# Kernel optimization log

Measured on AMD Instinct MI355X. Metric: run time of the kernel, lower is better.

Reference implementation:

```python
import jax, jax.numpy as jnp
import numpy as np

D_MODEL = 512
N_HEADS = 8
HEAD_DIM = D_MODEL // N_HEADS
SEQ = 2048
BATCH = 2
EPS = 1e-5
SCALE = 1.0 / np.sqrt(HEAD_DIM).astype(np.float32)
# (kind, window, dilation) per head, matching init_kwargs head_specs
SPECS = [("global", 0, 1), ("global", 0, 1),
         ("window", 64, 1), ("window", 128, 1), ("window", 256, 1),
         ("dilated", 64, 2), ("dilated", 64, 4), ("dilated", 64, 8)]


def build_masks(N):
    i = jnp.arange(N)
    D = jnp.abs(i[:, None] - i[None, :])
    ms = []
    for kind, w, dil in SPECS:
        if kind == "global":
            ms.append(jnp.ones((N, N), dtype=bool))
        elif kind == "window":
            ms.append(D <= w)
        else:  # dilated
            ms.append((D % dil == 0) & (D // dil <= w))
    return jnp.stack(ms)  # [H, N, N] bool


def layernorm(x, g, b):
    mu = jnp.mean(x, axis=-1, keepdims=True)
    var = jnp.mean((x - mu) ** 2, axis=-1, keepdims=True)
    return (x - mu) * jax.lax.rsqrt(var + EPS) * g + b


def setup_inputs() -> dict:
    key = jax.random.key(0)
    ks = jax.random.split(key, 7)
    w = 0.02
    return {
        "x": jax.random.normal(ks[0], (BATCH, SEQ, D_MODEL), dtype=jnp.float32),
        "Wq": jax.random.normal(ks[1], (D_MODEL, D_MODEL), dtype=jnp.float32) * w,
        "Wk": jax.random.normal(ks[2], (D_MODEL, D_MODEL), dtype=jnp.float32) * w,
        "Wv": jax.random.normal(ks[3], (D_MODEL, D_MODEL), dtype=jnp.float32) * w,
        "Wo": jax.random.normal(ks[4], (D_MODEL, D_MODEL), dtype=jnp.float32) * w,
        "T_w1": jax.random.normal(ks[5], (D_MODEL, D_MODEL), dtype=jnp.float32) * w,
        "T_b1": jnp.zeros((D_MODEL,), dtype=jnp.float32),
        "T_w2": jax.random.normal(ks[6], (1, D_MODEL), dtype=jnp.float32) * w,
        "T_b2": jnp.zeros((1,), dtype=jnp.float32),
        "ln_in_g": jnp.ones((D_MODEL,), dtype=jnp.float32),
        "ln_in_b": jnp.zeros((D_MODEL,), dtype=jnp.float32),
        "ln_out_g": jnp.ones((D_MODEL,), dtype=jnp.float32),
        "ln_out_b": jnp.zeros((D_MODEL,), dtype=jnp.float32),
    }


def reference(x, Wq, Wk, Wv, Wo, T_w1, T_b1, T_w2, T_b2,
              ln_in_g, ln_in_b, ln_out_g, ln_out_b):
    B, N, H = x.shape
    x0 = x
    xn = layernorm(x, ln_in_g, ln_in_b)
    # torch Linear: y = x @ W.T ; reshape to [B, h, N, d]
    def heads(W):
        return (xn @ W.T).reshape(B, N, N_HEADS, HEAD_DIM).transpose(0, 2, 1, 3)
    Q, K, V = heads(Wq), heads(Wk), heads(Wv)
    attn = jnp.einsum("bhqd,bhkd->bhqk", Q, K) * SCALE
    mask = build_masks(N)  # [h, N, N]
    attn = jnp.where(mask[None], attn, -jnp.inf)
    attn = jax.nn.softmax(attn, axis=-1)  # every row has diagonal unmasked
    out = jnp.einsum("bhqk,bhkd->bhqd", attn, V)
    out = out.transpose(0, 2, 1, 3).reshape(B, N, N_HEADS * HEAD_DIM)
    out = out @ Wo.T
    # tanh-gated softmax over sequence dim
    T_logits = jnp.tanh(xn @ T_w1.T + T_b1) @ T_w2.T + T_b2  # [B, N, 1]
    T = jax.nn.softmax(T_logits, axis=1)
    out = out * T
    return layernorm(out + x0, ln_out_g, ln_out_b)
```

## Files before the change

kernel.cpp:

```cpp
#include <hip/hip_runtime.h>
#include <math.h>

#define N_SEQ 2048
#define DM    512
#define NTOK  4096
#define NH    8
#define HD    64
#define NSLOT 18

typedef __attribute__((ext_vector_type(8))) short short8;
typedef __attribute__((ext_vector_type(4))) short short4_t;
typedef __attribute__((ext_vector_type(4))) float f32x4;

__device__ inline short f2bf(float x) {
    union { float f; unsigned u; } v; v.f = x;
    unsigned r = v.u + 0x7fff + ((v.u >> 16) & 1);
    return (short)(r >> 16);
}
__device__ inline float bf2f(short s) {
    union { unsigned u; float f; } v; v.u = ((unsigned)(unsigned short)s) << 16;
    return v.f;
}
__device__ inline unsigned pkbf(float a, float b) {
    return ((unsigned)(unsigned short)f2bf(b) << 16) | (unsigned)(unsigned short)f2bf(a);
}
__device__ inline float ftanh(float x) {
    float e = __expf(2.f * x);
    return 1.f - 2.f / (e + 1.f);
}

__device__ inline f32x4 mfma16(short8 a, short8 b, f32x4 c) {
    return __builtin_amdgcn_mfma_f32_16x16x32_bf16(a, b, c, 0, 0, 0);
}

__device__ __forceinline__ void async_cp16(const short* g, short* l) {
    __builtin_amdgcn_global_load_lds(
        (const __attribute__((address_space(1))) void*)g,
        (__attribute__((address_space(3))) void*)l, 16, 0, 0);
}

__global__ __launch_bounds__(256) void k_lncvt(
    const float* __restrict__ x, const float* __restrict__ g,
    const float* __restrict__ b, short* __restrict__ y, float* __restrict__ lg,
    const float* __restrict__ Wq, const float* __restrict__ Wk,
    const float* __restrict__ Wv, const float* __restrict__ Tw1,
    const float* __restrict__ Wo,
    short* __restrict__ wcat, short* __restrict__ wo) {
    int blk = blockIdx.x, t = threadIdx.x;
    if (blk < 2048) {
        int sub = t >> 7, tt = t & 127;
        int tk = blk * 2 + sub;
        if (tt == 0) lg[tk] = 0.f;
        float4 xv = ((const float4*)(x + (size_t)tk * DM))[tt];
        float s = xv.x + xv.y + xv.z + xv.w;
        float q = xv.x*xv.x + xv.y*xv.y + xv.z*xv.z + xv.w*xv.w;
        for (int o = 32; o; o >>= 1) { s += __shfl_down(s, o); q += __shfl_down(q, o); }
        __shared__ float ls[4], lq[4];
        if ((t & 63) == 0) { ls[t >> 6] = s; lq[t >> 6] = q; }
        __syncthreads();
        s = ls[sub * 2] + ls[sub * 2 + 1];
        q = lq[sub * 2] + lq[sub * 2 + 1];
        float mu = s * (1.f / DM);
        float var = q * (1.f / DM) - mu * mu;
        float rs = rsqrtf(var + 1e-5f);
        float4 gv = ((const float4*)g)[tt], bv = ((const float4*)b)[tt];
        short4_t o;
        o[0] = f2bf((xv.x - mu) * rs * gv.x + bv.x);
        o[1] = f2bf((xv.y - mu) * rs * gv.y + bv.y);
        o[2] = f2bf((xv.z - mu) * rs * gv.z + bv.z);
        o[3] = f2bf((xv.w - mu) * rs * gv.w + bv.w);
        *(short4_t*)&y[(size_t)tk * DM + tt * 4] = o;
    } else {
        int id = (blk - 2048) * 256 + t;
        if (id < 262144) {
            int z = id >> 16; int off = id & 65535;
            const float* s = (z == 0) ? Wq : (z == 1) ? Wk : (z == 2) ? Wv : Tw1;
            float4 v = ((const float4*)s)[off];
            short4_t o = {f2bf(v.x), f2bf(v.y), f2bf(v.z), f2bf(v.w)};
            *(short4_t*)(wcat + (size_t)z * 262144 + (size_t)off * 4) = o;
        } else {
            int off = id - 262144;
            float4 v = ((const float4*)Wo)[off];
            short4_t o = {f2bf(v.x), f2bf(v.y), f2bf(v.z), f2bf(v.w)};
            *(short4_t*)(wo + (size_t)off * 4) = o;
        }
    }
}

__global__ __launch_bounds__(256) void k_gemmqkvt(
    const short* __restrict__ A, const short* __restrict__ W,
    const float* __restrict__ Tb1, const float* __restrict__ Tw2,
    short* __restrict__ qb, short* __restrict__ kb, short* __restrict__ vtb,
    float* __restrict__ lg) {
    __shared__ short smem[17408];
    int t = threadIdx.x;
    int lane = t & 63, w = t >> 6;
    int wy = w >> 1, wx = w & 1;
    int ln = lane & 15, q4 = lane >> 4;
    int c0 = blockIdx.x * 128, m0 = blockIdx.y * 128;
    int sr = t >> 2, sc = (t & 3) << 3;
    f32x4 acc[4][4];
    f32x4 zero = {0.f, 0.f, 0.f, 0.f};
    #pragma unroll
    for (int i = 0; i < 4; i++)
        #pragma unroll
        for (int j = 0; j < 4; j++) acc[i][j] = zero;
    {
        short* AsB = smem; short* BsB = smem + 4096;
        async_cp16(&A[(size_t)(m0 + sr) * DM + sc],      &AsB[sr * 32 + sc]);
        async_cp16(&A[(size_t)(m0 + 64 + sr) * DM + sc], &AsB[(64 + sr) * 32 + sc]);
        async_cp16(&W[(size_t)(c0 + sr) * DM + sc],      &BsB[sr * 32 + sc]);
        async_cp16(&W[(size_t)(c0 + 64 + sr) * DM + sc], &BsB[(64 + sr) * 32 + sc]);
    }
    __syncthreads();
    for (int kk = 0; kk < 16; kk++) {
        short* AsB = &smem[(kk & 1) * 8192];
        short* BsB = AsB + 4096;
        if (kk < 15) {
            short* AsN = &smem[((kk & 1) ^ 1) * 8192];
            short* BsN = AsN + 4096;
            int k0 = (kk + 1) * 32;
            async_cp16(&A[(size_t)(m0 + sr) * DM + k0 + sc],      &AsN[sr * 32 + sc]);
            async_cp16(&A[(size_t)(m0 + 64 + sr) * DM + k0 + sc], &AsN[(64 + sr) * 32 + sc]);
            async_cp16(&W[(size_t)(c0 + sr) * DM + k0 + sc],      &BsN[sr * 32 + sc]);
            async_cp16(&W[(size_t)(c0 + 64 + sr) * DM + k0 + sc], &BsN[(64 + sr) * 32 + sc]);
        }
        short8 af[4], bfr[4];
        #pragma unroll
        for (int i = 0; i < 4; i++)
            af[i] = *(short8*)&AsB[(wy * 64 + i * 16 + ln) * 32 + q4 * 8];
        #pragma unroll
        for (int j = 0; j < 4; j++)
            bfr[j] = *(short8*)&BsB[(wx * 64 + j * 16 + ln) * 32 + q4 * 8];
        #pragma unroll
        for (int i = 0; i < 4; i++)
            #pragma unroll
            for (int j = 0; j < 4; j++)
                acc[i][j] = mfma16(af[i], bfr[j], acc[i][j]);
        __syncthreads();
    }
    short* Es = smem;
    int z = c0 >> 9;
    int bi = m0 >> 11, n0 = m0 & (N_SEQ - 1);
    int hp = (c0 & 511) >> 6;
    if (z < 2) {
        short* dst0 = (z == 0) ? qb : kb;
        float sc2 = (z == 0) ? 0.125f : 1.0f;
        #pragma unroll
        for (int i = 0; i < 4; i++)
            #pragma unroll
            for (int j = 0; j < 4; j++)
                #pragma unroll
                for (int r = 0; r < 4; r++) {
                    int nl = wy * 64 + i * 16 + q4 * 4 + r;
                    int cl = wx * 64 + j * 16 + ln;
                    Es[nl * 136 + cl] = f2bf(acc[i][j][r] * sc2);
                }
        __syncthreads();
        #pragma unroll
        for (int ii = 0; ii < 8; ii++) {
            int id = t + 256 * ii;
            int nl = id >> 4, c8 = id & 15;
            short8 v = *(short8*)&Es[nl * 136 + c8 * 8];
            int hh = hp + (c8 >> 3), d8 = (c8 & 7) * 8;
            *(short8*)&dst0[(((size_t)bi * NH + hh) * N_SEQ + n0 + nl) * HD + d8] = v;
        }
    } else if (z == 2) {
        #pragma unroll
        for (int i = 0; i < 4; i++)
            #pragma unroll
            for (int j = 0; j < 4; j++) {
                int nl0 = wy * 64 + i * 16 + q4 * 4;
                int dl = wx * 64 + j * 16 + ln;
                *(unsigned*)&Es[dl * 136 + nl0]     = pkbf(acc[i][j][0], acc[i][j][1]);
                *(unsigned*)&Es[dl * 136 + nl0 + 2] = pkbf(acc[i][j][2], acc[i][j][3]);
            }
        __syncthreads();
        #pragma unroll
        for (int ii = 0; ii < 8; ii++) {
            int id = t + 256 * ii;
            int dl = id >> 4, nc = id & 15;
            short8 v = *(short8*)&Es[dl * 136 + nc * 8];
            int h = hp + (dl >> 6), d = dl & 63;
            *(short8*)&vtb[(((size_t)bi * NH + h) * HD + d) * N_SEQ + n0 + nc * 8] = v;
        }
    } else {
        #pragma unroll
        for (int i = 0; i < 4; i++) {
            #pragma unroll
            for (int r = 0; r < 4; r++) {
                float s = 0.f;
                #pragma unroll
                for (int j = 0; j < 4; j++) {
                    int tc = (c0 & 511) + wx * 64 + j * 16 + ln;
                    s += ftanh(acc[i][j][r] + Tb1[tc]) * Tw2[tc];
                }
                s += __shfl_xor(s, 1);
                s += __shfl_xor(s, 2);
                s += __shfl_xor(s, 4);
                s += __shfl_xor(s, 8);
                if (ln == 0) {
                    int row = m0 + wy * 64 + i * 16 + q4 * 4 + r;
                    atomicAdd(&lg[row], s);
                }
            }
        }
    }
}

__global__ __launch_bounds__(256) void k_gemmp(
    const short* __restrict__ A, const short* __restrict__ W,
    float* __restrict__ proj) {
    __shared__ short smem[12288];
    int t = threadIdx.x;
    int lane = t & 63, w = t >> 6;
    int wy = w >> 1, wx = w & 1;
    int ln = lane & 15, q4 = lane >> 4;
    int c0 = blockIdx.x * 64, m0 = blockIdx.y * 128;
    int sr = t >> 2, sc = (t & 3) << 3;
    f32x4 acc[4][2];
    f32x4 zero = {0.f, 0.f, 0.f, 0.f};
    #pragma unroll
    for (int i = 0; i < 4; i++) { acc[i][0] = zero; acc[i][1] = zero; }
    {
        short* AsB = smem; short* BsB = smem + 4096;
        async_cp16(&A[(size_t)(m0 + sr) * DM + sc],      &AsB[sr * 32 + sc]);
        async_cp16(&A[(size_t)(m0 + 64 + sr) * DM + sc], &AsB[(64 + sr) * 32 + sc]);
        async_cp16(&W[(size_t)(c0 + sr) * DM + sc],      &BsB[sr * 32 + sc]);
    }
    __syncthreads();
    for (int kk = 0; kk < 16; kk++) {
        short* AsB = &smem[(kk & 1) * 6144];
        short* BsB = AsB + 4096;
        if (kk < 15) {
            short* AsN = &smem[((kk & 1) ^ 1) * 6144];
            short* BsN = AsN + 4096;
            int k0 = (kk + 1) * 32;
            async_cp16(&A[(size_t)(m0 + sr) * DM + k0 + sc],      &AsN[sr * 32 + sc]);
            async_cp16(&A[(size_t)(m0 + 64 + sr) * DM + k0 + sc], &AsN[(64 + sr) * 32 + sc]);
            async_cp16(&W[(size_t)(c0 + sr) * DM + k0 + sc],      &BsN[sr * 32 + sc]);
        }
        short8 af[4], bfr[2];
        #pragma unroll
        for (int i = 0; i < 4; i++)
            af[i] = *(short8*)&AsB[(wy * 64 + i * 16 + ln) * 32 + q4 * 8];
        #pragma unroll
        for (int j = 0; j < 2; j++)
            bfr[j] = *(short8*)&BsB[(wx * 32 + j * 16 + ln) * 32 + q4 * 8];
        #pragma unroll
        for (int i = 0; i < 4; i++)
            #pragma unroll
            for (int j = 0; j < 2; j++)
                acc[i][j] = mfma16(af[i], bfr[j], acc[i][j]);
        __syncthreads();
    }
    #pragma unroll
    for (int i = 0; i < 4; i++)
        #pragma unroll
        for (int j = 0; j < 2; j++)
            #pragma unroll
            for (int r = 0; r < 4; r++) {
                int row = m0 + wy * 64 + i * 16 + q4 * 4 + r;
                int col = c0 + wx * 32 + j * 16 + ln;
                proj[(size_t)row * DM + col] = acc[i][j][r];
            }
}

__global__ __launch_bounds__(256) void k_attn(const short* __restrict__ qb,
                                              const short* __restrict__ kb,
                                              const short* __restrict__ vtb,
                                              short* __restrict__ P_O,
                                              float* __restrict__ P_ml,
                                              short* __restrict__ ob,
                                              const float* __restrict__ lg,
                                              float* __restrict__ gate) {
    __shared__ short Ks[128 * 64];
    __shared__ short Vt[64 * 128];
    __shared__ short Pa[4][16 * 136];
    __shared__ float rg[8];
    int t = threadIdx.x;
    int lane = t & 63, w = t >> 6;
    int ln = lane & 15, q4 = lane >> 4;
    int slot = blockIdx.x, qt = blockIdx.y, bi = blockIdx.z;
    int q0 = qt * 64;
    int h, c;
    if (slot < 4)        { h = 0; c = slot; }
    else if (slot < 8)   { h = 1; c = slot - 4; }
    else if (slot == 8)  { h = 2; c = 0; }
    else if (slot == 9)  { h = 3; c = 0; }
    else if (slot < 12)  { h = 4; c = slot - 10; }
    else if (slot == 12) { h = 5; c = 0; }
    else if (slot < 15)  { h = 6; c = slot - 13; }
    else                 { h = 7; c = slot - 15; }
    int solo = (slot == 8) | (slot == 9) | (slot == 12);
    int kind = (h < 2) ? 0 : (h < 5) ? 1 : 2;
    int wnd = (h == 2 || h >= 5) ? 64 : (h == 3) ? 128 : (h == 4) ? 256 : 0;
    int dsh = (h == 5) ? 1 : (h == 6) ? 2 : (h == 7) ? 3 : 0;
    int dmask = (1 << dsh) - 1;
    int wmax = (kind == 0) ? 0 : (wnd << dsh);
    int tLoU, tHiU, CS;
    if (kind == 0) { tLoU = 0; tHiU = 15; CS = 4; }
    else { tLoU = (q0 - wmax) >> 7; tHiU = (q0 + 63 + wmax) >> 7; CS = 3; }
    int ktLo = tLoU + c * CS;
    int ktHi = ktLo + CS - 1;
    if (ktHi > tHiU) ktHi = tHiU;
    if (ktHi > 15) ktHi = 15;
    if (ktLo < 0) ktLo = 0;
    int p4 = (bi * 32 + qt) * NSLOT + slot;
    float* ml = P_ml + (size_t)p4 * 128;
    if (ktLo > ktHi) {
        if (t < 64) { ml[t] = -1e30f; ml[64 + t] = 0.f; }
        return;
    }
    const size_t base = ((size_t)bi * NH + h) * N_SEQ * HD;
    const short* Q = qb + base;
    const short* K = kb + base;
    const short* Vg = vtb + base;
    short8 qa[2];
    {
        const short* qrow = Q + (size_t)(q0 + w * 16 + ln) * HD + q4 * 8;
        qa[0] = *(const short8*)qrow;
        qa[1] = *(const short8*)(qrow + 32);
    }
    int qi = q0 + w * 16 + ln;
    float m_i = -1e30f, l_i = 0.f;
    f32x4 OT[4];
    f32x4 zero = {0.f, 0.f, 0.f, 0.f};
    #pragma unroll
    for (int d = 0; d < 4; d++) OT[d] = zero;
    short* Paw = Pa[w];
    for (int kt = ktLo; kt <= ktHi; kt++) {
        int k0 = kt << 7;
        __syncthreads();
        #pragma unroll
        for (int i2 = 0; i2 < 4; i2++) {
            int id = t + 256 * i2;
            int kr = id >> 3, ck = id & 7;
            async_cp16(&K[(size_t)(k0 + kr) * HD + ((ck ^ (kr & 7)) << 3)],
                       &Ks[id << 3]);
            int dr = id >> 4, cv = id & 15;
            async_cp16(&Vg[(size_t)dr * N_SEQ + k0 + ((cv ^ (dr & 15)) << 3)],
                       &Vt[id << 3]);
        }
        __syncthreads();
        f32x4 ST[8];
        #pragma unroll
        for (int nt = 0; nt < 8; nt++) ST[nt] = zero;
        __builtin_amdgcn_s_setprio(1);
        #pragma unroll
        for (int nt = 0; nt < 8; nt++) {
            #pragma unroll
            for (int ks = 0; ks < 2; ks++) {
                int cc = ((ks * 4 + q4) ^ (ln & 7)) << 3;
                short8 af = *(short8*)&Ks[(nt * 16 + ln) * 64 + cc];
                ST[nt] = mfma16(af, qa[ks], ST[nt]);
            }
        }
        __builtin_amdgcn_s_setprio(0);
        if (kind != 0) {
            #pragma unroll
            for (int nt = 0; nt < 8; nt++)
                #pragma unroll
                for (int r = 0; r < 4; r++) {
                    int key = k0 + nt * 16 + q4 * 4 + r;
                    int dlt = qi - key; dlt = (dlt < 0) ? -dlt : dlt;
                    int valid;
                    if (kind == 1) valid = (dlt <= wnd);
                    else valid = ((dlt & dmask) == 0) && ((dlt >> dsh) <= wnd);
                    if (!valid) ST[nt][r] = -1e30f;
                }
        }
        float rm = -1e30f;
        #pragma unroll
        for (int nt = 0; nt < 8; nt++) {
            float a = fmaxf(ST[nt][0], ST[nt][1]);
            float b = fmaxf(ST[nt][2], ST[nt][3]);
            rm = fmaxf(rm, fmaxf(a, b));
        }
        rm = fmaxf(rm, __shfl_xor(rm, 16));
        rm = fmaxf(rm, __shfl_xor(rm, 32));
        float mn = fmaxf(m_i, rm);
        float sc = __expf(m_i - mn);
        float rs = 0.f;
        #pragma unroll
        for (int nt = 0; nt < 8; nt++) {
            float p0 = __expf(ST[nt][0] - mn);
            float p1 = __expf(ST[nt][1] - mn);
            float p2 = __expf(ST[nt][2] - mn);
            float p3 = __expf(ST[nt][3] - mn);
            rs += (p0 + p1) + (p2 + p3);
            *(unsigned*)&Paw[ln * 136 + nt * 16 + q4 * 4]     = pkbf(p0, p1);
            *(unsigned*)&Paw[ln * 136 + nt * 16 + q4 * 4 + 2] = pkbf(p2, p3);
        }
        rs += __shfl_xor(rs, 16);
        rs += __shfl_xor(rs, 32);
        l_i = l_i * sc + rs;
        m_i = mn;
        #pragma unroll
        for (int d = 0; d < 4; d++) OT[d] *= sc;
        short8 pb[4];
        #pragma unroll
        for (int ks = 0; ks < 4; ks++)
            pb[ks] = *(short8*)&Paw[ln * 136 + ks * 32 + q4 * 8];
        __builtin_amdgcn_s_setprio(1);
        #pragma unroll
        for (int dt = 0; dt < 4; dt++) {
            #pragma unroll
            for (int ks = 0; ks < 4; ks++) {
                int cc = ((ks * 4 + q4) ^ ln) << 3;
                short8 a = *(short8*)&Vt[(dt * 16 + ln) * 128 + cc];
                OT[dt] = mfma16(a, pb[ks], OT[dt]);
            }
        }
        __builtin_amdgcn_s_setprio(0);
    }
    if (solo) {
        float inv = 1.f / l_i;
        #pragma unroll
        for (int dt = 0; dt < 4; dt++) {
            *(unsigned*)&Paw[ln * 136 + dt * 16 + q4 * 4]     = pkbf(OT[dt][0] * inv, OT[dt][1] * inv);
            *(unsigned*)&Paw[ln * 136 + dt * 16 + q4 * 4 + 2] = pkbf(OT[dt][2] * inv, OT[dt][3] * inv);
        }
        short8 o0 = *(short8*)&Paw[ln * 136 + q4 * 16];
        short8 o1 = *(short8*)&Paw[ln * 136 + q4 * 16 + 8];
        short* dst = ob + ((size_t)bi * N_SEQ + q0 + w * 16 + ln) * DM + h * 64 + q4 * 16;
        *(short8*)dst = o0;
        *(short8*)(dst + 8) = o1;
    } else {
        if (q4 == 0) { ml[w * 16 + ln] = m_i; ml[64 + w * 16 + ln] = l_i; }
        #pragma unroll
        for (int dt = 0; dt < 4; dt++) {
            *(unsigned*)&Paw[ln * 136 + dt * 16 + q4 * 4]     = pkbf(OT[dt][0], OT[dt][1]);
            *(unsigned*)&Paw[ln * 136 + dt * 16 + q4 * 4 + 2] = pkbf(OT[dt][2], OT[dt][3]);
        }
        short8 o0 = *(short8*)&Paw[ln * 136 + q4 * 16];
        short8 o1 = *(short8*)&Paw[ln * 136 + q4 * 16 + 8];
        short* Op = P_O + (size_t)p4 * 4096;
        *(short8*)&Op[(w * 16 + ln) * 64 + q4 * 16] = o0;
        *(short8*)&Op[(w * 16 + ln) * 64 + q4 * 16 + 8] = o1;
    }
    if (slot == 8 && qt == 0) {
        int b = bi;
        float v[8];
        float4 a0 = *(const float4*)&lg[b * N_SEQ + t * 8];
        float4 a1 = *(const float4*)&lg[b * N_SEQ + t * 8 + 4];
        v[0] = a0.x; v[1] = a0.y; v[2] = a0.z; v[3] = a0.w;
        v[4] = a1.x; v[5] = a1.y; v[6] = a1.z; v[7] = a1.w;
        float m = v[0];
        #pragma unroll
        for (int j = 1; j < 8; j++) m = fmaxf(m, v[j]);
        for (int o = 32; o; o >>= 1) m = fmaxf(m, __shfl_down(m, o));
        if ((t & 63) == 0) rg[t >> 6] = m;
        __syncthreads();
        m = fmaxf(fmaxf(rg[0], rg[1]), fmaxf(rg[2], rg[3]));
        float e[8], s = 0.f;
        #pragma unroll
        for (int j = 0; j < 8; j++) { e[j] = __expf(v[j] - m); s += e[j]; }
        for (int o = 32; o; o >>= 1) s += __shfl_down(s, o);
        if ((t & 63) == 0) rg[4 + (t >> 6)] = s;
        __syncthreads();
        s = (rg[4] + rg[5]) + (rg[6] + rg[7]);
        float inv = 1.f / s;
        float4 o0 = {e[0] * inv, e[1] * inv, e[2] * inv, e[3] * inv};
        float4 o1 = {e[4] * inv, e[5] * inv, e[6] * inv, e[7] * inv};
        *(float4*)&gate[b * N_SEQ + t * 8] = o0;
        *(float4*)&gate[b * N_SEQ + t * 8 + 4] = o1;
    }
}

__global__ __launch_bounds__(256) void k_combine(const short* __restrict__ P_O,
                                                 const float* __restrict__ P_ml,
                                                 short* __restrict__ ob) {
    const int hsel[5]  = {0, 1, 4, 6, 7};
    const int hbase[5] = {0, 4, 10, 13, 15};
    const int hcnt[5]  = {4, 4, 2, 2, 3};
    int hh = blockIdx.x, qt = blockIdx.y, bi = blockIdx.z;
    int h = hsel[hh];
    int t = threadIdx.x;
    int row = t >> 2, c0 = (t & 3) * 16;
    int pb = (bi * 32 + qt) * NSLOT + hbase[hh];
    int cnt = hcnt[hh];
    float m = -1e30f;
    for (int s = 0; s < cnt; s++)
        m = fmaxf(m, P_ml[(size_t)(pb + s) * 128 + row]);
    float l = 0.f;
    float acc[16];
    #pragma unroll
    for (int j = 0; j < 16; j++) acc[j] = 0.f;
    for (int s = 0; s < cnt; s++) {
        float ms = P_ml[(size_t)(pb + s) * 128 + row];
        float ls = P_ml[(size_t)(pb + s) * 128 + 64 + row];
        if (ls > 0.f) {
            float sc = __expf(ms - m);
            l += ls * sc;
            const short* Op = P_O + (size_t)(pb + s) * 4096 + row * 64 + c0;
            short8 v0 = *(const short8*)Op;
            short8 v1 = *(const short8*)(Op + 8);
            #pragma unroll
            for (int j = 0; j < 8; j++) acc[j]     += bf2f(v0[j]) * sc;
            #pragma unroll
            for (int j = 0; j < 8; j++) acc[8 + j] += bf2f(v1[j]) * sc;
        }
    }
    float inv = 1.f / l;
    int n = qt * 64 + row;
    short8 o0, o1;
    #pragma unroll
    for (int j = 0; j < 8; j++) o0[j] = f2bf(acc[j] * inv);
    #pragma unroll
    for (int j = 0; j < 8; j++) o1[j] = f2bf(acc[8 + j] * inv);
    short* dst = ob + ((size_t)bi * N_SEQ + n) * DM + h * 64 + c0;
    *(short8*)dst = o0;
    *(short8*)(dst + 8) = o1;
}

__global__ __launch_bounds__(128) void k_final(const float* __restrict__ proj,
                                               const float* __restrict__ gate,
                                               const float* __restrict__ x0,
                                               const float* __restrict__ g,
                                               const float* __restrict__ b,
                                               float* __restrict__ out) {
    int tk = blockIdx.x, t = threadIdx.x;
    float gt = gate[tk];
    float4 pv = ((const float4*)(proj + (size_t)tk * DM))[t];
    float4 xv = ((const float4*)(x0 + (size_t)tk * DM))[t];
    float4 y;
    y.x = pv.x * gt + xv.x;
    y.y = pv.y * gt + xv.y;
    y.z = pv.z * gt + xv.z;
    y.w = pv.w * gt + xv.w;
    float s = y.x + y.y + y.z + y.w;
    float q = y.x*y.x + y.y*y.y + y.z*y.z + y.w*y.w;
    for (int o = 32; o; o >>= 1) { s += __shfl_down(s, o); q += __shfl_down(q, o); }
    __shared__ float ls[2], lq[2];
    if ((t & 63) == 0) { ls[t >> 6] = s; lq[t >> 6] = q; }
    __syncthreads();
    s = ls[0] + ls[1]; q = lq[0] + lq[1];
    float mu = s * (1.f / DM);
    float var = q * (1.f / DM) - mu * mu;
    float rs = rsqrtf(var + 1e-5f);
    float4 gv = ((const float4*)g)[t], bv = ((const float4*)b)[t];
    float4 o;
    o.x = (y.x - mu) * rs * gv.x + bv.x;
    o.y = (y.y - mu) * rs * gv.y + bv.y;
    o.z = (y.z - mu) * rs * gv.z + bv.z;
    o.w = (y.w - mu) * rs * gv.w + bv.w;
    ((float4*)(out + (size_t)tk * DM))[t] = o;
}

extern "C" void kernel_launch(void* const* d_in, const int* in_sizes, int n_in,
                              void* d_out, int out_size, void* d_ws, size_t ws_size,
                              hipStream_t stream) {
    (void)in_sizes; (void)n_in; (void)out_size; (void)ws_size;
    const float* x    = (const float*)d_in[0];
    const float* Wq   = (const float*)d_in[1];
    const float* Wk   = (const float*)d_in[2];
    const float* Wv   = (const float*)d_in[3];
    const float* Wo   = (const float*)d_in[4];
    const float* Tw1  = (const float*)d_in[5];
    const float* Tb1  = (const float*)d_in[6];
    const float* Tw2  = (const float*)d_in[7];
    const float* ling = (const float*)d_in[9];
    const float* linb = (const float*)d_in[10];
    const float* logg = (const float*)d_in[11];
    const float* logb = (const float*)d_in[12];
    float* out = (float*)d_out;

    const size_t SZ = (size_t)NTOK * DM;
    const int NPART = 2 * 32 * NSLOT;
    char* p = (char*)d_ws;
    short* xn   = (short*)p; p += SZ * 2;
    short* wcat = (short*)p; p += (size_t)2048 * DM * 2;
    short* wo   = (short*)p; p += (size_t)DM * DM * 2;
    short* qb   = (short*)p; p += SZ * 2;
    short* kb   = (short*)p; p += SZ * 2;
    short* vtb  = (short*)p; p += SZ * 2;
    short* obuf = (short*)p; p += SZ * 2;
    float* lg   = (float*)p; p += (size_t)NTOK * 4;
    float* gate = (float*)p; p += (size_t)NTOK * 4;
    float* P_ml = (float*)p; p += (size_t)NPART * 128 * 4;
    float* proj = (float*)p;
    short* P_O  = (short*)p; p += (size_t)NPART * 4096 * 2;

    k_lncvt<<<3328, 256, 0, stream>>>(x, ling, linb, xn, lg,
                                      Wq, Wk, Wv, Tw1, Wo, wcat, wo);
    k_gemmqkvt<<<dim3(16, 32), 256, 0, stream>>>(xn, wcat, Tb1, Tw2,
                                                 qb, kb, vtb, lg);
    k_attn<<<dim3(NSLOT, 32, 2), 256, 0, stream>>>(qb, kb, vtb, P_O, P_ml,
                                                   obuf, lg, gate);
    k_combine<<<dim3(5, 32, 2), 256, 0, stream>>>(P_O, P_ml, obuf);
    k_gemmp<<<dim3(8, 32), 256, 0, stream>>>(obuf, wo, proj);
    k_final<<<NTOK, 128, 0, stream>>>(proj, gate, x, logg, logb, out);
}
```

Measured before the change: 154.5 us.

## Fuse split-KV combine into output projection GEMM, drop solo-slot direct writes

After: 167.9 us. +8.7%, slower.

```diff
diff --git a/kernel.cpp b/kernel.cpp
--- a/kernel.cpp
+++ b/kernel.cpp
@@ -208,70 +208,11 @@
     }
 }
 
-__global__ __launch_bounds__(256) void k_gemmp(
-    const short* __restrict__ A, const short* __restrict__ W,
-    float* __restrict__ proj) {
-    __shared__ short smem[12288];
-    int t = threadIdx.x;
-    int lane = t & 63, w = t >> 6;
-    int wy = w >> 1, wx = w & 1;
-    int ln = lane & 15, q4 = lane >> 4;
-    int c0 = blockIdx.x * 64, m0 = blockIdx.y * 128;
-    int sr = t >> 2, sc = (t & 3) << 3;
-    f32x4 acc[4][2];
-    f32x4 zero = {0.f, 0.f, 0.f, 0.f};
-    #pragma unroll
-    for (int i = 0; i < 4; i++) { acc[i][0] = zero; acc[i][1] = zero; }
-    {
-        short* AsB = smem; short* BsB = smem + 4096;
-        async_cp16(&A[(size_t)(m0 + sr) * DM + sc],      &AsB[sr * 32 + sc]);
-        async_cp16(&A[(size_t)(m0 + 64 + sr) * DM + sc], &AsB[(64 + sr) * 32 + sc]);
-        async_cp16(&W[(size_t)(c0 + sr) * DM + sc],      &BsB[sr * 32 + sc]);
-    }
-    __syncthreads();
-    for (int kk = 0; kk < 16; kk++) {
-        short* AsB = &smem[(kk & 1) * 6144];
-        short* BsB = AsB + 4096;
-        if (kk < 15) {
-            short* AsN = &smem[((kk & 1) ^ 1) * 6144];
-            short* BsN = AsN + 4096;
-            int k0 = (kk + 1) * 32;
-            async_cp16(&A[(size_t)(m0 + sr) * DM + k0 + sc],      &AsN[sr * 32 + sc]);
-            async_cp16(&A[(size_t)(m0 + 64 + sr) * DM + k0 + sc], &AsN[(64 + sr) * 32 + sc]);
-            async_cp16(&W[(size_t)(c0 + sr) * DM + k0 + sc],      &BsN[sr * 32 + sc]);
-        }
-        short8 af[4], bfr[2];
-        #pragma unroll
-        for (int i = 0; i < 4; i++)
-            af[i] = *(short8*)&AsB[(wy * 64 + i * 16 + ln) * 32 + q4 * 8];
-        #pragma unroll
-        for (int j = 0; j < 2; j++)
-            bfr[j] = *(short8*)&BsB[(wx * 32 + j * 16 + ln) * 32 + q4 * 8];
-        #pragma unroll
-        for (int i = 0; i < 4; i++)
-            #pragma unroll
-            for (int j = 0; j < 2; j++)
-                acc[i][j] = mfma16(af[i], bfr[j], acc[i][j]);
-        __syncthreads();
-    }
-    #pragma unroll
-    for (int i = 0; i < 4; i++)
-        #pragma unroll
-        for (int j = 0; j < 2; j++)
-            #pragma unroll
-            for (int r = 0; r < 4; r++) {
-                int row = m0 + wy * 64 + i * 16 + q4 * 4 + r;
-                int col = c0 + wx * 32 + j * 16 + ln;
-                proj[(size_t)row * DM + col] = acc[i][j][r];
-            }
-}
-
 __global__ __launch_bounds__(256) void k_attn(const short* __restrict__ qb,
                                               const short* __restrict__ kb,
                                               const short* __restrict__ vtb,
                                               short* __restrict__ P_O,
                                               float* __restrict__ P_ml,
-                                              short* __restrict__ ob,
                                               const float* __restrict__ lg,
                                               float* __restrict__ gate) {
     __shared__ short Ks[128 * 64];
@@ -292,7 +233,6 @@
     else if (slot == 12) { h = 5; c = 0; }
     else if (slot < 15)  { h = 6; c = slot - 13; }
     else                 { h = 7; c = slot - 15; }
-    int solo = (slot == 8) | (slot == 9) | (slot == 12);
     int kind = (h < 2) ? 0 : (h < 5) ? 1 : 2;
     int wnd = (h == 2 || h >= 5) ? 64 : (h == 3) ? 128 : (h == 4) ? 256 : 0;
     int dsh = (h == 5) ? 1 : (h == 6) ? 2 : (h == 7) ? 3 : 0;
@@ -308,125 +248,114 @@
     if (ktLo < 0) ktLo = 0;
     int p4 = (bi * 32 + qt) * NSLOT + slot;
     float* ml = P_ml + (size_t)p4 * 128;
-    if (ktLo > ktHi) {
+    int empty = (ktLo > ktHi);
+    if (empty) {
         if (t < 64) { ml[t] = -1e30f; ml[64 + t] = 0.f; }
-        return;
+        if (!(slot == 8 && qt == 0)) return;
     }
     const size_t base = ((size_t)bi * NH + h) * N_SEQ * HD;
     const short* Q = qb + base;
     const short* K = kb + base;
     const short* Vg = vtb + base;
-    short8 qa[2];
-    {
-        const short* qrow = Q + (size_t)(q0 + w * 16 + ln) * HD + q4 * 8;
-        qa[0] = *(const short8*)qrow;
-        qa[1] = *(const short8*)(qrow + 32);
-    }
-    int qi = q0 + w * 16 + ln;
-    float m_i = -1e30f, l_i = 0.f;
-    f32x4 OT[4];
-    f32x4 zero = {0.f, 0.f, 0.f, 0.f};
-    #pragma unroll
-    for (int d = 0; d < 4; d++) OT[d] = zero;
-    short* Paw = Pa[w];
-    for (int kt = ktLo; kt <= ktHi; kt++) {
-        int k0 = kt << 7;
-        __syncthreads();
-        #pragma unroll
-        for (int i2 = 0; i2 < 4; i2++) {
-            int id = t + 256 * i2;
-            int kr = id >> 3, ck = id & 7;
-            async_cp16(&K[(size_t)(k0 + kr) * HD + ((ck ^ (kr & 7)) << 3)],
-                       &Ks[id << 3]);
-            int dr = id >> 4, cv = id & 15;
-            async_cp16(&Vg[(size_t)dr * N_SEQ + k0 + ((cv ^ (dr & 15)) << 3)],
-                       &Vt[id << 3]);
-        }
-        __syncthreads();
-        f32x4 ST[8];
-        #pragma unroll
-        for (int nt = 0; nt < 8; nt++) ST[nt] = zero;
-        __builtin_amdgcn_s_setprio(1);
-        #pragma unroll
-        for (int nt = 0; nt < 8; nt++) {
-            #pragma unroll
-            for (int ks = 0; ks < 2; ks++) {
-                int cc = ((ks * 4 + q4) ^ (ln & 7)) << 3;
-                short8 af = *(short8*)&Ks[(nt * 16 + ln) * 64 + cc];
-                ST[nt] = mfma16(af, qa[ks], ST[nt]);
-            }
-        }
-        __builtin_amdgcn_s_setprio(0);
-        if (kind != 0) {
-            #pragma unroll
-            for (int nt = 0; nt < 8; nt++)
+    if (!empty) {
+        short8 qa[2];
+        {
+            const short* qrow = Q + (size_t)(q0 + w * 16 + ln) * HD + q4 * 8;
+            qa[0] = *(const short8*)qrow;
+            qa[1] = *(const short8*)(qrow + 32);
+        }
+        int qi = q0 + w * 16 + ln;
+        float m_i = -1e30f, l_i = 0.f;
+        f32x4 OT[4];
+        f32x4 zero = {0.f, 0.f, 0.f, 0.f};
+        #pragma unroll
+        for (int d = 0; d < 4; d++) OT[d] = zero;
+        short* Paw = Pa[w];
+        for (int kt = ktLo; kt <= ktHi; kt++) {
+            int k0 = kt << 7;
+            __syncthreads();
+            #pragma unroll
+            for (int i2 = 0; i2 < 4; i2++) {
+                int id = t + 256 * i2;
+                int kr = id >> 3, ck = id & 7;
+                async_cp16(&K[(size_t)(k0 + kr) * HD + ((ck ^ (kr & 7)) << 3)],
+                           &Ks[id << 3]);
+                int dr = id >> 4, cv = id & 15;
+                async_cp16(&Vg[(size_t)dr * N_SEQ + k0 + ((cv ^ (dr & 15)) << 3)],
+                           &Vt[id << 3]);
+            }
+            __syncthreads();
+            f32x4 ST[8];
+            #pragma unroll
+            for (int nt = 0; nt < 8; nt++) ST[nt] = zero;
+            __builtin_amdgcn_s_setprio(1);
+            #pragma unroll
+            for (int nt = 0; nt < 8; nt++) {
                 #pragma unroll
-                for (int r = 0; r < 4; r++) {
-                    int key = k0 + nt * 16 + q4 * 4 + r;
-                    int dlt = qi - key; dlt = (dlt < 0) ? -dlt : dlt;
-                    int valid;
-                    if (kind == 1) valid = (dlt <= wnd);
-                    else valid = ((dlt & dmask) == 0) && ((dlt >> dsh) <= wnd);
-                    if (!valid) ST[nt][r] = -1e30f;
+                for (int ks = 0; ks < 2; ks++) {
+                    int cc = ((ks * 4 + q4) ^ (ln & 7)) << 3;
+                    short8 af = *(short8*)&Ks[(nt * 16 + ln) * 64 + cc];
+                    ST[nt] = mfma16(af, qa[ks], ST[nt]);
                 }
-        }
-        float rm = -1e30f;
-        #pragma unroll
-        for (int nt = 0; nt < 8; nt++) {
-            float a = fmaxf(ST[nt][0], ST[nt][1]);
-            float b = fmaxf(ST[nt][2], ST[nt][3]);
-            rm = fmaxf(rm, fmaxf(a, b));
-        }
-        rm = fmaxf(rm, __shfl_xor(rm, 16));
-        rm = fmaxf(rm, __shfl_xor(rm, 32));
-        float mn = fmaxf(m_i, rm);
-        float sc = __expf(m_i - mn);
-        float rs = 0.f;
-        #pragma unroll
-        for (int nt = 0; nt < 8; nt++) {
-            float p0 = __expf(ST[nt][0] - mn);
-            float p1 = __expf(ST[nt][1] - mn);
-            float p2 = __expf(ST[nt][2] - mn);
-            float p3 = __expf(ST[nt][3] - mn);
-            rs += (p0 + p1) + (p2 + p3);
-            *(unsigned*)&Paw[ln * 136 + nt * 16 + q4 * 4]     = pkbf(p0, p1);
-            *(unsigned*)&Paw[ln * 136 + nt * 16 + q4 * 4 + 2] = pkbf(p2, p3);
-        }
-        rs += __shfl_xor(rs, 16);
-        rs += __shfl_xor(rs, 32);
-        l_i = l_i * sc + rs;
-        m_i = mn;
-        #pragma unroll
-        for (int d = 0; d < 4; d++) OT[d] *= sc;
-        short8 pb[4];
-        #pragma unroll
-        for (int ks = 0; ks < 4; ks++)
-            pb[ks] = *(short8*)&Paw[ln * 136 + ks * 32 + q4 * 8];
-        __builtin_amdgcn_s_setprio(1);
-        #pragma unroll
-        for (int dt = 0; dt < 4; dt++) {
-            #pragma unroll
-            for (int ks = 0; ks < 4; ks++) {
-                int cc = ((ks * 4 + q4) ^ ln) << 3;
-                short8 a = *(short8*)&Vt[(dt * 16 + ln) * 128 + cc];
-                OT[dt] = mfma16(a, pb[ks], OT[dt]);
-            }
-        }
-        __builtin_amdgcn_s_setprio(0);
-    }
-    if (solo) {
-        float inv = 1.f / l_i;
-        #pragma unroll
-        for (int dt = 0; dt < 4; dt++) {
-            *(unsigned*)&Paw[ln * 136 + dt * 16 + q4 * 4]     = pkbf(OT[dt][0] * inv, OT[dt][1] * inv);
-            *(unsigned*)&Paw[ln * 136 + dt * 16 + q4 * 4 + 2] = pkbf(OT[dt][2] * inv, OT[dt][3] * inv);
-        }
-        short8 o0 = *(short8*)&Paw[ln * 136 + q4 * 16];
-        short8 o1 = *(short8*)&Paw[ln * 136 + q4 * 16 + 8];
-        short* dst = ob + ((size_t)bi * N_SEQ + q0 + w * 16 + ln) * DM + h * 64 + q4 * 16;
-        *(short8*)dst = o0;
-        *(short8*)(dst + 8) = o1;
-    } else {
+            }
+            __builtin_amdgcn_s_setprio(0);
+            if (kind != 0) {
+                #pragma unroll
+                for (int nt = 0; nt < 8; nt++)
+                    #pragma unroll
+                    for (int r = 0; r < 4; r++) {
+                        int key = k0 + nt * 16 + q4 * 4 + r;
+                        int dlt = qi - key; dlt = (dlt < 0) ? -dlt : dlt;
+                        int valid;
+                        if (kind == 1) valid = (dlt <= wnd);
+                        else valid = ((dlt & dmask) == 0) && ((dlt >> dsh) <= wnd);
+                        if (!valid) ST[nt][r] = -1e30f;
+                    }
+            }
+            float rm = -1e30f;
+            #pragma unroll
+            for (int nt = 0; nt < 8; nt++) {
+                float a = fmaxf(ST[nt][0], ST[nt][1]);
+                float b = fmaxf(ST[nt][2], ST[nt][3]);
+                rm = fmaxf(rm, fmaxf(a, b));
+            }
+            rm = fmaxf(rm, __shfl_xor(rm, 16));
+            rm = fmaxf(rm, __shfl_xor(rm, 32));
+            float mn = fmaxf(m_i, rm);
+            float sc = __expf(m_i - mn);
+            float rs = 0.f;
+            #pragma unroll
+            for (int nt = 0; nt < 8; nt++) {
+                float p0 = __expf(ST[nt][0] - mn);
+                float p1 = __expf(ST[nt][1] - mn);
+                float p2 = __expf(ST[nt][2] - mn);
+                float p3 = __expf(ST[nt][3] - mn);
+                rs += (p0 + p1) + (p2 + p3);
+                *(unsigned*)&Paw[ln * 136 + nt * 16 + q4 * 4]     = pkbf(p0, p1);
+                *(unsigned*)&Paw[ln * 136 + nt * 16 + q4 * 4 + 2] = pkbf(p2, p3);
+            }
+            rs += __shfl_xor(rs, 16);
+            rs += __shfl_xor(rs, 32);
+            l_i = l_i * sc + rs;
+            m_i = mn;
+            #pragma unroll
+            for (int d = 0; d < 4; d++) OT[d] *= sc;
+            short8 pb[4];
+            #pragma unroll
+            for (int ks = 0; ks < 4; ks++)
+                pb[ks] = *(short8*)&Paw[ln * 136 + ks * 32 + q4 * 8];
+            __builtin_amdgcn_s_setprio(1);
+            #pragma unroll
+            for (int dt = 0; dt < 4; dt++) {
+                #pragma unroll
+                for (int ks = 0; ks < 4; ks++) {
+                    int cc = ((ks * 4 + q4) ^ ln) << 3;
+                    short8 a = *(short8*)&Vt[(dt * 16 + ln) * 128 + cc];
+                    OT[dt] = mfma16(a, pb[ks], OT[dt]);
+                }
+            }
+            __builtin_amdgcn_s_setprio(0);
+        }
         if (q4 == 0) { ml[w * 16 + ln] = m_i; ml[64 + w * 16 + ln] = l_i; }
         #pragma unroll
         for (int dt = 0; dt < 4; dt++) {
@@ -468,50 +397,100 @@
     }
 }
 
-__global__ __launch_bounds__(256) void k_combine(const short* __restrict__ P_O,
-                                                 const float* __restrict__ P_ml,
-                                                 short* __restrict__ ob) {
-    const int hsel[5]  = {0, 1, 4, 6, 7};
-    const int hbase[5] = {0, 4, 10, 13, 15};
-    const int hcnt[5]  = {4, 4, 2, 2, 3};
-    int hh = blockIdx.x, qt = blockIdx.y, bi = blockIdx.z;
-    int h = hsel[hh];
+__global__ __launch_bounds__(256) void k_cproj(
+    const short* __restrict__ P_O, const float* __restrict__ P_ml,
+    const short* __restrict__ wo, float* __restrict__ proj) {
+    __shared__ short As[64 * 512];
+    __shared__ short Bs[2][128 * 32];
     int t = threadIdx.x;
-    int row = t >> 2, c0 = (t & 3) * 16;
-    int pb = (bi * 32 + qt) * NSLOT + hbase[hh];
-    int cnt = hcnt[hh];
-    float m = -1e30f;
-    for (int s = 0; s < cnt; s++)
-        m = fmaxf(m, P_ml[(size_t)(pb + s) * 128 + row]);
-    float l = 0.f;
-    float acc[16];
+    int lane = t & 63, w = t >> 6;
+    int ln = lane & 15, q4 = lane >> 4;
+    int c0 = blockIdx.x * 128;
+    int m0 = blockIdx.y * 64;
+    int bi = m0 >> 11, qt = (m0 & 2047) >> 6;
+    const int hbase[8] = {0, 4, 8, 9, 10, 12, 13, 15};
+    const int hcnt[8]  = {4, 4, 1, 1, 2, 1, 2, 3};
+    int pbb = (bi * 32 + qt) * NSLOT;
     #pragma unroll
-    for (int j = 0; j < 16; j++) acc[j] = 0.f;
-    for (int s = 0; s < cnt; s++) {
-        float ms = P_ml[(size_t)(pb + s) * 128 + row];
-        float ls = P_ml[(size_t)(pb + s) * 128 + 64 + row];
-        if (ls > 0.f) {
-            float sc = __expf(ms - m);
-            l += ls * sc;
-            const short* Op = P_O + (size_t)(pb + s) * 4096 + row * 64 + c0;
-            short8 v0 = *(const short8*)Op;
-            short8 v1 = *(const short8*)(Op + 8);
-            #pragma unroll
-            for (int j = 0; j < 8; j++) acc[j]     += bf2f(v0[j]) * sc;
-            #pragma unroll
-            for (int j = 0; j < 8; j++) acc[8 + j] += bf2f(v1[j]) * sc;
-        }
-    }
-    float inv = 1.f / l;
-    int n = qt * 64 + row;
-    short8 o0, o1;
+    for (int i2 = 0; i2 < 2; i2++) {
+        int id = t + 256 * i2;
+        int row = id >> 2, cc = id & 3;
+        async_cp16(&wo[(size_t)(c0 + row) * DM + ((cc ^ (row & 3)) << 3)],
+                   &Bs[0][id * 8]);
+    }
     #pragma unroll
-    for (int j = 0; j < 8; j++) o0[j] = f2bf(acc[j] * inv);
+    for (int ii = 0; ii < 2; ii++) {
+        int id = t + 256 * ii;
+        int row = id >> 3, c8 = id & 7;
+        #pragma unroll
+        for (int h = 0; h < 8; h++) {
+            int pb = pbb + hbase[h], cnt = hcnt[h];
+            float m = -1e30f;
+            for (int s = 0; s < cnt; s++)
+                m = fmaxf(m, P_ml[(size_t)(pb + s) * 128 + row]);
+            float l = 0.f;
+            float a8[8];
+            #pragma unroll
+            for (int j = 0; j < 8; j++) a8[j] = 0.f;
+            for (int s = 0; s < cnt; s++) {
+                float ms = P_ml[(size_t)(pb + s) * 128 + row];
+                float ls = P_ml[(size_t)(pb + s) * 128 + 64 + row];
+                if (ls > 0.f) {
+                    float sc = __expf(ms - m);
+                    l += ls * sc;
+                    short8 v = *(const short8*)&P_O[(size_t)(pb + s) * 4096 + row * 64 + c8 * 8];
+                    #pragma unroll
+                    for (int j = 0; j < 8; j++) a8[j] += bf2f(v[j]) * sc;
+                }
+            }
+            float inv = 1.f / l;
+            short8 o;
+            #pragma unroll
+            for (int j = 0; j < 8; j++) o[j] = f2bf(a8[j] * inv);
+            int chunk = (h << 3) | (c8 ^ (row & 7));
+            *(short8*)&As[row * 512 + chunk * 8] = o;
+        }
+    }
+    __syncthreads();
+    f32x4 acc[8];
+    f32x4 zero = {0.f, 0.f, 0.f, 0.f};
     #pragma unroll
-    for (int j = 0; j < 8; j++) o1[j] = f2bf(acc[8 + j] * inv);
-    short* dst = ob + ((size_t)bi * N_SEQ + n) * DM + h * 64 + c0;
-    *(short8*)dst = o0;
-    *(short8*)(dst + 8) = o1;
+    for (int j = 0; j < 8; j++) acc[j] = zero;
+    for (int kk = 0; kk < 16; kk++) {
+        short* BsB = Bs[kk & 1];
+        if (kk < 15) {
+            int k0 = (kk + 1) * 32;
+            short* BsN = Bs[(kk & 1) ^ 1];
+            #pragma unroll
+            for (int i2 = 0; i2 < 2; i2++) {
+                int id = t + 256 * i2;
+                int row = id >> 2, cc = id & 3;
+                async_cp16(&wo[(size_t)(c0 + row) * DM + k0 + ((cc ^ (row & 3)) << 3)],
+                           &BsN[id * 8]);
+            }
+        }
+        int r2 = w * 16 + ln;
+        int chunk = (kk * 4 + q4) ^ (r2 & 7);
+        short8 af = *(short8*)&As[r2 * 512 + chunk * 8];
+        short8 bfr[8];
+        #pragma unroll
+        for (int j = 0; j < 8; j++) {
+            int br = j * 16 + ln;
+            bfr[j] = *(short8*)&BsB[br * 32 + ((q4 ^ (br & 3)) << 3)];
+        }
+        #pragma unroll
+        for (int j = 0; j < 8; j++)
+            acc[j] = mfma16(af, bfr[j], acc[j]);
+        __syncthreads();
+    }
+    #pragma unroll
+    for (int j = 0; j < 8; j++)
+        #pragma unroll
+        for (int r = 0; r < 4; r++) {
+            int row = m0 + w * 16 + q4 * 4 + r;
+            int col = c0 + j * 16 + ln;
+            proj[(size_t)row * DM + col] = acc[j][r];
+        }
 }
 
 __global__ __launch_bounds__(128) void k_final(const float* __restrict__ proj,
@@ -575,20 +554,18 @@
     short* qb   = (short*)p; p += SZ * 2;
     short* kb   = (short*)p; p += SZ * 2;
     short* vtb  = (short*)p; p += SZ * 2;
-    short* obuf = (short*)p; p += SZ * 2;
     float* lg   = (float*)p; p += (size_t)NTOK * 4;
     float* gate = (float*)p; p += (size_t)NTOK * 4;
     float* P_ml = (float*)p; p += (size_t)NPART * 128 * 4;
-    float* proj = (float*)p;
     short* P_O  = (short*)p; p += (size_t)NPART * 4096 * 2;
+    float* proj = (float*)p; p += SZ * 4;
 
     k_lncvt<<<3328, 256, 0, stream>>>(x, ling, linb, xn, lg,
                                       Wq, Wk, Wv, Tw1, Wo, wcat, wo);
     k_gemmqkvt<<<dim3(16, 32), 256, 0, stream>>>(xn, wcat, Tb1, Tw2,
                                                  qb, kb, vtb, lg);
     k_attn<<<dim3(NSLOT, 32, 2), 256, 0, stream>>>(qb, kb, vtb, P_O, P_ml,
-                                                   obuf, lg, gate);
-    k_combine<<<dim3(5, 32, 2), 256, 0, stream>>>(P_O, P_ml, obuf);
-    k_gemmp<<<dim3(8, 32), 256, 0, stream>>>(obuf, wo, proj);
+                                                   lg, gate);
+    k_cproj<<<dim3(4, 64), 256, 0, stream>>>(P_O, P_ml, wo, proj);
     k_final<<<NTOK, 128, 0, stream>>>(proj, gate, x, logg, logb, out);
 }
```
